# Kernel tuning notes

Hardware: AMD Instinct MI355X
Metric: run time of the kernel (lower is better)

Reference implementation:

```python
import jax, jax.numpy as jnp
import numpy as np

D = 1024
H = 16
HD = D // H
FF = 4096
B, S = 2, 2048


def _ln(x, g, b, eps):
    mu = jnp.mean(x, axis=-1, keepdims=True)
    var = jnp.mean(jnp.square(x - mu), axis=-1, keepdims=True)
    return (x - mu) * jax.lax.rsqrt(var + eps) * g + b


def setup_inputs() -> dict:
    key = jax.random.key(0)
    ks = jax.random.split(key, 12)
    s = 0.02
    return {
        "x": jax.random.normal(ks[0], (B, S, D), jnp.float32),
        "attention_mask": jnp.ones((B, 1, 1, S), jnp.int32),
        "wq": jax.random.normal(ks[1], (D, D), jnp.float32) * s,
        "bq": jnp.zeros((D,), jnp.float32),
        "wk": jax.random.normal(ks[2], (D, D), jnp.float32) * s,
        "bk": jnp.zeros((D,), jnp.float32),
        "wv": jax.random.normal(ks[3], (D, D), jnp.float32) * s,
        "bv": jnp.zeros((D,), jnp.float32),
        "wo": jax.random.normal(ks[4], (D, D), jnp.float32) * s,
        "bo": jnp.zeros((D,), jnp.float32),
        "ln1_g": jnp.ones((D,), jnp.float32),
        "ln1_b": jnp.zeros((D,), jnp.float32),
        "w1": jax.random.normal(ks[5], (D, FF), jnp.float32) * s,
        "b1": jnp.zeros((FF,), jnp.float32),
        "w2": jax.random.normal(ks[6], (FF, D), jnp.float32) * s,
        "b2": jnp.zeros((D,), jnp.float32),
        "lnf_g": jnp.ones((D,), jnp.float32),
        "lnf_b": jnp.zeros((D,), jnp.float32),
        "ln2_g": jnp.ones((D,), jnp.float32),
        "ln2_b": jnp.zeros((D,), jnp.float32),
    }


def reference(x, attention_mask, wq, bq, wk, bk, wv, bv, wo, bo,
              ln1_g, ln1_b, w1, b1, w2, b2, lnf_g, lnf_b, ln2_g, ln2_b):
    b, s, d = x.shape
    # --- naive multi-head self-attention ---
    q = (x @ wq + bq).reshape(b, s, H, HD).transpose(0, 2, 1, 3)  # [b,h,s,hd]
    k = (x @ wk + bk).reshape(b, s, H, HD).transpose(0, 2, 1, 3)
    v = (x @ wv + bv).reshape(b, s, H, HD).transpose(0, 2, 1, 3)
    scores = jnp.einsum('bhqd,bhkd->bhqk', q, k) / jnp.sqrt(jnp.float32(HD))
    scores = jnp.where(attention_mask == 0, jnp.float32(-1e9), scores)
    attn = jax.nn.softmax(scores, axis=-1)
    ctx = jnp.einsum('bhqk,bhkd->bhqd', attn, v)
    ctx = ctx.transpose(0, 2, 1, 3).reshape(b, s, d)
    attn_out = ctx @ wo + bo
    # residual + LayerNorm (eps=1e-5, torch default)
    x1 = _ln(x + attn_out, ln1_g, ln1_b, 1e-5)
    # --- BERT-style FFN with internal residual LN (eps=1e-12) ---
    h = jax.nn.gelu(x1 @ w1 + b1, approximate=False)
    ff = _ln(h @ w2 + b2 + x1, lnf_g, lnf_b, 1e-12)
    # --- outer residual + LayerNorm (eps=1e-5) ---
    return _ln(x1 + ff, ln2_g, ln2_b, 1e-5)
```

## Files before the change

kernel.cpp:

```cpp
#include <hip/hip_runtime.h>

#define DMODEL 1024
#define NHEAD  16
#define HDIM   64
#define FFDIM  4096
#define BATCH  2
#define SEQ    2048
#define MTOK   (BATCH*SEQ)

typedef __bf16 bf16;
typedef __bf16 bf16x8 __attribute__((ext_vector_type(8)));
typedef __bf16 bf16x4 __attribute__((ext_vector_type(4)));
typedef float  floatx4 __attribute__((ext_vector_type(4)));
typedef unsigned int u32;
typedef unsigned int u32x4 __attribute__((ext_vector_type(4)));

__device__ __forceinline__ int get_flag(const void* ln1g) {
  return (((const u32*)ln1g)[0] == 0x3F800000u) ? 0 : 1;
}
__device__ __forceinline__ float ld_ext(const void* p, size_t i, int flag) {
  return flag ? (float)((const bf16*)p)[i] : ((const float*)p)[i];
}

__device__ __forceinline__ void gload16(const bf16* g, bf16* lds_uniform) {
// ... 35 lines not shown
  }
  if (bid >= 12288) {
    size_t base = (size_t)(bid - 12288) * 1024;
    int i = threadIdx.x * 4;
    #pragma unroll
    for (int j = 0; j < 4; j++) xC[base + i + j] = (bf16)ld_ext(x, base + i + j, flag);
    return;
  }
  __shared__ bf16 tile[32][33];
  const void* in; bf16* out; int K, N, t;
  if      (bid < 1024)  { in = wq; out = WTqkv;                 K = 1024; N = 1024; t = bid; }
  else if (bid < 2048)  { in = wk; out = WTqkv + 1024 * 1024;   K = 1024; N = 1024; t = bid - 1024; }
  else if (bid < 3072)  { in = wv; out = WTqkv + 2 * 1024 * 1024; K = 1024; N = 1024; t = bid - 2048; }
  else if (bid < 4096)  { in = wo; out = WToT;                  K = 1024; N = 1024; t = bid - 3072; }
  else if (bid < 8192)  { in = w1; out = WT1;                   K = 1024; N = 4096; t = bid - 4096; }
  else                  { in = w2; out = WT2;                   K = 4096; N = 1024; t = bid - 8192; }
  int shift = (N == 4096) ? 7 : 5;
  int k0 = (t >> shift) * 32, n0 = (t & ((1 << shift) - 1)) * 32;
  int tx = threadIdx.x & 31, ty = threadIdx.x >> 5;
  #pragma unroll
  for (int i = ty; i < 32; i += 8)
    tile[i][tx] = (bf16)ld_ext(in, (size_t)(k0 + i) * N + n0 + tx, flag);
  __syncthreads();
  #pragma unroll
  for (int i = ty; i < 32; i += 8)
    out[(size_t)(n0 + i) * K + k0 + tx] = tile[tx][i];
}

__global__ __launch_bounds__(256) void gemm128(
    const bf16* __restrict__ A, const bf16* __restrict__ BT,
    const void* __restrict__ bias0, const void* __restrict__ bias1,
    const void* __restrict__ bias2,
    bf16* __restrict__ out0, bf16* __restrict__ out1, bf16* __restrict__ out2,
    int N, int K, int ksub, int mode, const void* __restrict__ ln1g)
{
  __shared__ __align__(16) char smem[32768];
  bf16* As = (bf16*)smem;
  bf16* Bs = (bf16*)(smem + 16384);
  int flag = get_flag(ln1g);

  int tid = threadIdx.x, lane = tid & 63, w = tid >> 6;
  int wm = w & 1, wn = w >> 1;
  int m0 = blockIdx.x * 128, n0 = blockIdx.y * 128;
  int kstart = blockIdx.z * ksub;
  int r15 = lane & 15, kg = lane >> 4;

  floatx4 acc[4][4];
  #pragma unroll
  for (int mt = 0; mt < 4; mt++)
    #pragma unroll
    for (int nt = 0; nt < 4; nt++) acc[mt][nt] = (floatx4){0.f, 0.f, 0.f, 0.f};

  int srow8 = lane >> 3;
  int skc = (lane & 7) ^ (srow8 & 7);
  const bf16* Ap = A  + (size_t)(m0 + w * 32 + srow8) * K + kstart + skc * 8;
  const bf16* Bp = BT + (size_t)(n0 + w * 32 + srow8) * K + kstart + skc * 8;
  const size_t jstr = (size_t)8 * K;

  for (int it = ksub >> 6; it > 0; it--) {
    #pragma unroll
    for (int j = 0; j < 4; j++) {
      gload16(Ap + j * jstr, As + (size_t)(w * 256 + j * 64) * 8);
      gload16(Bp + j * jstr, Bs + (size_t)(w * 256 + j * 64) * 8);
    }
    Ap += 64; Bp += 64;
    __syncthreads();

// ... 32 lines not shown
  for (int nt = 0; nt < 4; nt++) {
    int gcol = gcb + nt * 16 + r15;
    int bidx = (mode == 1) ? (gcol & 1023) : gcol;
    const void* bp = (mode == 1) ? ((which == 0) ? bias0 : (which == 1) ? bias1 : bias2) : bias0;
    bvs[nt] = (blockIdx.z == 0) ? ld_ext(bp, bidx, flag) : 0.f;
  }

  #pragma unroll
  for (int pass = 0; pass < 2; pass++) {
    #pragma unroll
    for (int mh = 0; mh < 2; mh++) {
      int mt = 2 * pass + mh;
      #pragma unroll
      for (int nt = 0; nt < 4; nt++) {
        int lcol = nt * 16 + r15;
        #pragma unroll
        for (int r = 0; r < 4; r++) {
          int lrow = mh * 16 + kg * 4 + r;
          float val = acc[mt][nt][r] + bvs[nt];
          if (mode == 2) val = gelu_f(val);
          if (mode == 1 && which == 0) val *= 0.125f;
          if (mode == 1 && which == 2) scr[lcol * 40 + lrow] = (bf16)val;
          else                         scr[lrow * 68 + lcol] = (bf16)val;
        }
      }
    }
    if (mode == 1 && which == 2) {
      int hh = (gcb - 2048) >> 6;
      int b = rowg0 >> 11, s0 = rowg0 & 2047;
      #pragma unroll
      for (int it = 0; it < 4; it++) {
        int c = it * 64 + lane;
        int cc = c >> 2, part = c & 3;
        bf16x8 vdat = *(const bf16x8*)&scr[cc * 40 + part * 8];
        *(bf16x8*)(out2 + ((size_t)(b * NHEAD + hh) * HDIM + cc) * SEQ + s0 + pass * 32 + part * 8) = vdat;
      }
    } else {
      #pragma unroll
      for (int it = 0; it < 4; it++) {
        int c = it * 64 + lane;
        int rr = c >> 3, part = c & 7;
        bf16x8 vdat = *(const bf16x8*)&scr[rr * 68 + part * 8];
        int rowg = rowg0 + pass * 32 + rr;
        bf16* dst;
        if (mode == 1) {
          int b = rowg >> 11, s = rowg & 2047;
          int hh = (gcb & 1023) >> 6;
          bf16* o = (which == 0) ? out0 : out1;
          dst = o + ((size_t)(b * NHEAD + hh) * SEQ + s) * HDIM + part * 8;
        } else {
          dst = outp + (size_t)rowg * N + gcb + part * 8;
        }
        *(bf16x8*)dst = vdat;
      }
    }
  }
}

#define STAGE_A(dstbuf, koff, qm)                                             \
  { int gch = (lane & 7) ^ (srow8 & 7);                                       \
    _Pragma("unroll") for (int j = 0; j < 2; j++) {                           \
      int rb = (qm) * 64 + j * 128 + w * 8;                                   \
      gload16(A + (size_t)(m0 + rb + srow8) * K + (koff) + gch * 8,           \
              (dstbuf) + (size_t)rb * 64);                                    \
    } }

#define STAGE_B(dstbuf, koff, qn)                                             \
  { int gch = (lane & 7) ^ (srow8 & 7);                                       \
    _Pragma("unroll") for (int j = 0; j < 2; j++) {                           \
      int rb = (2 * j + (w >> 2)) * 64 + (qn) * 32 + (w & 3) * 8;             \
      gload16(BT + (size_t)(n0 + rb + srow8) * K + (koff) + gch * 8,          \
              (dstbuf) + (size_t)rb * 64);                                    \
    } }

#define RD_A(QM)                                                              \
  _Pragma("unroll") for (int mt = 0; mt < 4; mt++) {                          \
    int row = wm * 128 + (QM) * 64 + mt * 16 + r15;                           \
    _Pragma("unroll") for (int kk = 0; kk < 2; kk++) {                        \
      int slot = (kk * 4 + kg) ^ (r15 & 7);                                   \
      af[mt][kk] = *(const bf16x8*)&Ac[(size_t)(row * 8 + slot) * 8];         \
    }                                                                         \
  }

#define RD_B(QN)                                                              \
  _Pragma("unroll") for (int nt = 0; nt < 2; nt++) {                          \
    int row = wn * 64 + (QN) * 32 + nt * 16 + r15;                            \
    _Pragma("unroll") for (int kk = 0; kk < 2; kk++) {                        \
      int slot = (kk * 4 + kg) ^ (r15 & 7);                                   \
      bfv[nt][kk] = *(const bf16x8*)&Bc[(size_t)(row * 8 + slot) * 8];        \
    }                                                                         \
  }

#define MF(QM, QN)                                                            \
  __builtin_amdgcn_s_setprio(1);                                              \
  _Pragma("unroll") for (int kk = 0; kk < 2; kk++)                            \
    _Pragma("unroll") for (int mt = 0; mt < 4; mt++)                          \
      _Pragma("unroll") for (int nt = 0; nt < 2; nt++)                        \
        acc[(QM) * 4 + mt][(QN) * 2 + nt] =                                   \
            __builtin_amdgcn_mfma_f32_16x16x32_bf16(                          \
                af[mt][kk], bfv[nt][kk],                                      \
                acc[(QM) * 4 + mt][(QN) * 2 + nt], 0, 0, 0);                  \
  __builtin_amdgcn_s_setprio(0);

__global__ __launch_bounds__(512, 2) void gemm256(
    const bf16* __restrict__ A, const bf16* __restrict__ BT,
    const void* __restrict__ bias0, bf16* __restrict__ out0,
    int N, int K, int ksub, int mode, const void* __restrict__ ln1g)
{
  __shared__ __align__(16) char smem[131072];
  int flag = get_flag(ln1g);

  int tid = threadIdx.x, lane = tid & 63, w = tid >> 6;
  int wm = w >> 2, wn = w & 3;
  int r15 = lane & 15, kg = lane >> 4;
  int srow8 = lane >> 3;

  int nx = gridDim.x, ny = gridDim.y;
  int nwg = nx * ny * gridDim.z;
  int wg = blockIdx.x + nx * (blockIdx.y + ny * blockIdx.z);
  if ((nwg & 7) == 0) wg = (wg & 7) * (nwg >> 3) + (wg >> 3);
  int bx = wg % nx, rem = wg / nx;
  int by = rem % ny, bz = rem / ny;

  int m0 = bx * 256, n0 = by * 256;
  int kstart = bz * ksub;
  int NT = ksub >> 6;

  floatx4 acc[8][4];
  #pragma unroll
  for (int mt = 0; mt < 8; mt++)
    #pragma unroll
    for (int nt = 0; nt < 4; nt++) acc[mt][nt] = (floatx4){0.f, 0.f, 0.f, 0.f};

  STAGE_A((bf16*)smem,             kstart, 0);
  STAGE_B((bf16*)(smem + 65536),   kstart, 0);
  STAGE_A((bf16*)smem,             kstart, 1);
  STAGE_B((bf16*)(smem + 65536),   kstart, 1);
  VMW(4);
  BAR();

  for (int t = 0; t < NT; t++) {
    int cur = (t & 1) * 32768, nxt = ((t + 1) & 1) * 32768;
    bf16* Ac = (bf16*)(smem + cur);
    bf16* Bc = (bf16*)(smem + 65536 + cur);
    bf16* An = (bf16*)(smem + nxt);
    bf16* Bn = (bf16*)(smem + 65536 + nxt);
    int t1 = (t + 1 < NT) ? t + 1 : NT - 1;
    int k1 = kstart + t1 * 64;

    bf16x8 af[4][2], bfv[2][2];
    RD_A(0); RD_B(0);
    STAGE_A(An, k1, 0);
    VMW(4);
    BAR(); MF(0, 0); BAR();
    RD_A(1);
    STAGE_B(Bn, k1, 0);
    VMW(4);
    BAR(); MF(1, 0); BAR();
    RD_B(1);
    STAGE_A(An, k1, 1);
    BAR(); MF(1, 1); BAR();
    RD_A(0);
    STAGE_B(Bn, k1, 1);
    VMW(4);
    BAR(); MF(0, 1); BAR();
  }

  VMW(0);
  BAR();

  bf16* scr = (bf16*)(smem + 5120 * w);
  int gcb = n0 + wn * 64;
  int rowg0 = m0 + wm * 128;
  bf16* outp = out0 + (size_t)bz * MTOK * (size_t)N;

  float bvs[4];
  #pragma unroll
  for (int nt = 0; nt < 4; nt++) {
    int gcol = gcb + nt * 16 + r15;
    bvs[nt] = (bz == 0) ? ld_ext(bias0, gcol, flag) : 0.f;
  }

  #pragma unroll
  for (int pass = 0; pass < 4; pass++) {
    #pragma unroll
    for (int mh = 0; mh < 2; mh++) {
      int mt = 2 * pass + mh;
      #pragma unroll
      for (int nt = 0; nt < 4; nt++) {
        #pragma unroll
        for (int r = 0; r < 4; r++) {
          int lrow = mh * 16 + kg * 4 + r;
          float val = acc[mt][nt][r] + bvs[nt];
          if (mode == 2) val = gelu_f(val);
          scr[lrow * 68 + nt * 16 + r15] = (bf16)val;
        }
      }
    }
    #pragma unroll
    for (int it = 0; it < 4; it++) {
      int c = it * 64 + lane;
      int rr = c >> 3, part = c & 7;
      bf16x8 vdat = *(const bf16x8*)&scr[rr * 68 + part * 8];
      int rowg = rowg0 + pass * 32 + rr;
      *(bf16x8*)(outp + (size_t)rowg * N + gcb + part * 8) = vdat;
    }
  }
}

__global__ __launch_bounds__(256) void attn_mfma(
    const bf16* __restrict__ q, const bf16* __restrict__ k,
    const bf16* __restrict__ vt, const u32* __restrict__ mwAll,
    const bf16* __restrict__ m01All, bf16* __restrict__ ctx)
{
  __shared__ __align__(16) bf16 Ks[2][4096];
  __shared__ __align__(16) bf16 Vts[2][4096];
  __shared__ __align__(16) bf16 Ps[4][2048];

  int tid = threadIdx.x, lane = tid & 63, w = tid >> 6;
  int r15 = lane & 15, kg = lane >> 4;
  int x7 = r15 & 7;
  int bh = (blockIdx.x & 7) * 4 + ((blockIdx.x >> 3) >> 4);
  int qt = (blockIdx.x >> 3) & 15;
  int b = bh >> 4, h = bh & 15;
  int q0 = qt * 128 + w * 32;

  bf16x8 qf[2][2];
  #pragma unroll
  for (int mt = 0; mt < 2; mt++)
    #pragma unroll
    for (int kt2 = 0; kt2 < 2; kt2++)
      qf[mt][kt2] = *(const bf16x8*)(q + ((size_t)bh * SEQ + q0 + mt * 16 + r15) * HDIM + kt2 * 32 + kg * 8);

  floatx4 O[2][4];
  floatx4 lacc[2];
  #pragma unroll
  for (int mt = 0; mt < 2; mt++) {
    lacc[mt] = (floatx4){0.f, 0.f, 0.f, 0.f};
    #pragma unroll
    for (int dt = 0; dt < 4; dt++) O[mt][dt] = (floatx4){0.f, 0.f, 0.f, 0.f};
  }

  int slo = kg ^ x7, shi = (kg + 4) ^ x7;
  const bf16* pap[2][2];
  #pragma unroll
  for (int mt = 0; mt < 2; mt++) {
    pap[mt][0] = &Ps[w][((mt * 16 + r15) * 8 + slo) * 8];
    pap[mt][1] = &Ps[w][((mt * 16 + r15) * 8 + shi) * 8];
  }

  int kr = lane >> 3, kc = lane & 7;
  int vrow = tid >> 3, vcc = tid & 7;
  int vsw = vcc ^ (vrow & 7);
  const bf16* kb_ = k + (size_t)bh * SEQ * HDIM;
  const bf16* vb_ = vt + (size_t)bh * HDIM * SEQ;
  const u32*  mwb = mwAll + (size_t)b * (SEQ / 2);
  const bf16* m1b = m01All + (size_t)b * SEQ;

  u32x4 pv0 = *(const u32x4*)(vb_ + (size_t)vrow * SEQ + vcc * 8);
  u32x4 pv1 = *(const u32x4*)(vb_ + (size_t)(vrow + 32) * SEQ + vcc * 8);
  u32x4 pmw = *(const u32x4*)&mwb[vcc * 4];
  bf16x8 m0c = *(const bf16x8*)&m1b[kg * 8];
  bf16x8 m1c = *(const bf16x8*)&m1b[32 + kg * 8];
  asm volatile("" ::: "memory");
  #pragma unroll
  for (int j = 0; j < 2; j++)
    gload16(kb_ + (size_t)(16 * w + 8 * j + kr) * HDIM + (kc ^ kr) * 8,
            &Ks[0][0] + (size_t)(w * 128 + j * 64) * 8);
  VMW(4);
  pv0 &= pmw; pv1 &= pmw;
  *(u32x4*)&Vts[0][(vrow * 8 + vsw) * 8] = pv0;
  *(u32x4*)&Vts[0][((vrow + 32) * 8 + vsw) * 8] = pv1;
  asm volatile("s_waitcnt lgkmcnt(0)" ::: "memory");
  __builtin_amdgcn_s_barrier();
  asm volatile("" ::: "memory");

  for (int t = 0; t < SEQ / 64; t++) {
    int cur = t & 1, nxt = cur ^ 1;
    int ktn = (t + 1 < SEQ / 64) ? (t + 1) * 64 : t * 64;
    u32x4 nv0 = *(const u32x4*)(vb_ + (size_t)vrow * SEQ + ktn + vcc * 8);
    u32x4 nv1 = *(const u32x4*)(vb_ + (size_t)(vrow + 32) * SEQ + ktn + vcc * 8);
    u32x4 nmw = *(const u32x4*)&mwb[(ktn + vcc * 8) >> 1];
    bf16x8 nm0 = *(const bf16x8*)&m1b[ktn + kg * 8];
    bf16x8 nm1 = *(const bf16x8*)&m1b[ktn + 32 + kg * 8];
    asm volatile("" ::: "memory");
    #pragma unroll
    for (int j = 0; j < 2; j++)
      gload16(kb_ + (size_t)(ktn + 16 * w + 8 * j + kr) * HDIM + (kc ^ kr) * 8,
              &Ks[nxt][0] + (size_t)(w * 128 + j * 64) * 8);
    VMW(7);
    __builtin_amdgcn_s_barrier();
    asm volatile("" ::: "memory");

    const bf16* Kc = &Ks[cur][0];
    const bf16* Vc = &Vts[cur][0];

    floatx4 S[2][4];
    #pragma unroll
    for (int mt = 0; mt < 2; mt++)
      #pragma unroll
      for (int nt = 0; nt < 4; nt++) S[mt][nt] = (floatx4){0.f, 0.f, 0.f, 0.f};
    __builtin_amdgcn_s_setprio(1);
    #pragma unroll
    for (int nt = 0; nt < 4; nt++) {
      int rb = (nt * 16 + r15) * 8;
      bf16x8 kf0 = *(const bf16x8*)&Kc[(rb + slo) * 8];
      bf16x8 kf1 = *(const bf16x8*)&Kc[(rb + shi) * 8];
      #pragma unroll
      for (int mt = 0; mt < 2; mt++) {
        S[mt][nt] = __builtin_amdgcn_mfma_f32_16x16x32_bf16(kf0, qf[mt][0], S[mt][nt], 0, 0, 0);
        S[mt][nt] = __builtin_amdgcn_mfma_f32_16x16x32_bf16(kf1, qf[mt][1], S[mt][nt], 0, 0, 0);
      }
    }
    __builtin_amdgcn_s_setprio(0);

    #pragma unroll
    for (int mt = 0; mt < 2; mt++)
      #pragma unroll
      for (int nt = 0; nt < 4; nt++) {
        bf16x4 pk;
        #pragma unroll
        for (int r = 0; r < 4; r++) pk[r] = (bf16)__expf(S[mt][nt][r]);
        int c2 = 2 * nt + (kg >> 1);
        *(bf16x4*)&Ps[w][((mt * 16 + r15) * 8 + (c2 ^ x7)) * 8 + (kg & 1) * 4] = pk;
      }

    bf16x8 pa[2][2];
    #pragma unroll
    for (int mt = 0; mt < 2; mt++) {
      pa[mt][0] = *(const bf16x8*)pap[mt][0];
      pa[mt][1] = *(const bf16x8*)pap[mt][1];
    }
    __builtin_amdgcn_s_setprio(1);
    #pragma unroll
    for (int dt = 0; dt < 4; dt++) {
      int rb = (dt * 16 + r15) * 8;
      bf16x8 vf0 = *(const bf16x8*)&Vc[(rb + slo) * 8];
      bf16x8 vf1 = *(const bf16x8*)&Vc[(rb + shi) * 8];
      #pragma unroll
      for (int mt = 0; mt < 2; mt++) {
        O[mt][dt] = __builtin_amdgcn_mfma_f32_16x16x32_bf16(pa[mt][0], vf0, O[mt][dt], 0, 0, 0);
        O[mt][dt] = __builtin_amdgcn_mfma_f32_16x16x32_bf16(pa[mt][1], vf1, O[mt][dt], 0, 0, 0);
      }
    }
    #pragma unroll
    for (int mt = 0; mt < 2; mt++) {
      lacc[mt] = __builtin_amdgcn_mfma_f32_16x16x32_bf16(pa[mt][0], m0c, lacc[mt], 0, 0, 0);
      lacc[mt] = __builtin_amdgcn_mfma_f32_16x16x32_bf16(pa[mt][1], m1c, lacc[mt], 0, 0, 0);
    }
    __builtin_amdgcn_s_setprio(0);

    VMW(2);
    nv0 &= nmw; nv1 &= nmw;
    *(u32x4*)&Vts[nxt][(vrow * 8 + vsw) * 8] = nv0;
    *(u32x4*)&Vts[nxt][((vrow + 32) * 8 + vsw) * 8] = nv1;
    m0c = nm0; m1c = nm1;
    asm volatile("s_waitcnt lgkmcnt(0)" ::: "memory");
    __builtin_amdgcn_s_barrier();
    asm volatile("" ::: "memory");
  }
  VMW(0);

  #pragma unroll
  for (int mt = 0; mt < 2; mt++) {
    float inv[4];
    #pragma unroll
    for (int r = 0; r < 4; r++) inv[r] = 1.f / lacc[mt][r];
    #pragma unroll
    for (int dt = 0; dt < 4; dt++)
      #pragma unroll
      for (int r = 0; r < 4; r++) {
        int srow = q0 + mt * 16 + kg * 4 + r;
        int col = h * 64 + dt * 16 + r15;
        ctx[((size_t)b * SEQ + srow) * DMODEL + col] = (bf16)(O[mt][dt][r] * inv[r]);
      }
  }
}

__global__ __launch_bounds__(256) void ln_kernel(
    const bf16* ba, const bf16* bb, const bf16* bc,
    const void* g, const void* be, float eps, bf16* outb, const void* ln1g)
{
  __shared__ float red1[4], red2[4];
  int flag = get_flag(ln1g);
  size_t base = (size_t)blockIdx.x * DMODEL;
  float v[4];
  #pragma unroll
  for (int i = 0; i < 4; i++) {
    int idx = threadIdx.x + i * 256;
    v[i] = (float)ba[base + idx] + (float)bb[base + idx] + (float)bc[base + idx];
  }
  float sum = v[0] + v[1] + v[2] + v[3];
  #pragma unroll
  for (int o = 32; o > 0; o >>= 1) sum += __shfl_xor(sum, o);
  if ((threadIdx.x & 63) == 0) red1[threadIdx.x >> 6] = sum;
  __syncthreads();
  float mean = (red1[0] + red1[1] + red1[2] + red1[3]) * (1.f / DMODEL);
  float sq = 0.f;
  #pragma unroll
  for (int i = 0; i < 4; i++) { v[i] -= mean; sq += v[i] * v[i]; }
  #pragma unroll
  for (int o = 32; o > 0; o >>= 1) sq += __shfl_xor(sq, o);
  if ((threadIdx.x & 63) == 0) red2[threadIdx.x >> 6] = sq;
  __syncthreads();
  float rstd = rsqrtf((red2[0] + red2[1] + red2[2] + red2[3]) * (1.f / DMODEL) + eps);
  #pragma unroll
  for (int i = 0; i < 4; i++) {
    int idx = threadIdx.x + i * 256;
    outb[base + idx] = (bf16)(v[i] * rstd * ld_ext(g, idx, flag) + ld_ext(be, idx, flag));
// ... 57 lines not shown
    int idx = threadIdx.x + i * 256;
    float y = v[i] * rstd * ld_ext(g2, idx, flag) + ld_ext(b2, idx, flag);
    if (flag) ((bf16*)out_ext)[base + idx] = (bf16)y;
    else      ((float*)out_ext)[base + idx] = y;
  }
}

extern "C" void kernel_launch(void* const* d_in, const int* in_sizes, int n_in,
                              void* d_out, int out_size, void* d_ws, size_t ws_size,
                              hipStream_t stream) {
  const void* x    = d_in[0];
  const int*  msk  = (const int*)d_in[1];
  const void* wq   = d_in[2];
  const void* bq   = d_in[3];
  const void* wk   = d_in[4];
  const void* bk   = d_in[5];
  const void* wv   = d_in[6];
  const void* bv   = d_in[7];
  const void* wo   = d_in[8];
  const void* bo   = d_in[9];
  const void* ln1g = d_in[10];
  const void* ln1b = d_in[11];
  const void* w1   = d_in[12];
  const void* b1   = d_in[13];
  const void* w2   = d_in[14];
  const void* b2   = d_in[15];
  const void* lnfg = d_in[16];
  const void* lnfb = d_in[17];
  const void* ln2g = d_in[18];
  const void* ln2b = d_in[19];

  const size_t MB = 1024 * 1024;
  char* p = (char*)d_ws;
  int big = ws_size >= (size_t)80 * MB;
  bf16* xC     = (bf16*)(p + 0 * MB);
  bf16* qb     = (bf16*)(p + 8 * MB);
  bf16* kb     = (bf16*)(p + 16 * MB);
  bf16* vtb    = (bf16*)(p + 24 * MB);
  bf16* ctxb   = (bf16*)(p + 32 * MB);
  bf16* WTqkv  = (bf16*)(p + 40 * MB);
  bf16* WToT   = (bf16*)(p + 46 * MB);
  bf16* WT1    = (bf16*)(p + 48 * MB);
  bf16* WT2    = (bf16*)(p + (big ? 72 : 56) * MB);
  bf16* ao     = (bf16*)(p + 8 * MB);
  bf16* x1b    = xC;
  bf16* hb     = (bf16*)(p + 8 * MB);
  bf16* ffp    = (bf16*)(p + 40 * MB);
  u32*  mwAll  = (u32*)d_out;
  bf16* m01All = (bf16*)((char*)d_out + 8192);
  const size_t PS = (size_t)MTOK * DMODEL;

  prep<<<16386, 256, 0, stream>>>(wq, wk, wv, wo, w1, w2, x, msk,
                                  WTqkv, WToT, WT1, WT2, xC, mwAll, m01All, ln1g);

  gemm128<<<dim3(MTOK / 128, 3072 / 128, 1), 256, 0, stream>>>(
      xC, WTqkv, bq, bk, bv, qb, kb, vtb, 3072, DMODEL, DMODEL, 1, ln1g);

  attn_mfma<<<BATCH * NHEAD * (SEQ / 128), 256, 0, stream>>>(qb, kb, vtb, mwAll, m01All, ctxb);

  gemm128<<<dim3(MTOK / 128, DMODEL / 128, 2), 256, 0, stream>>>(
      ctxb, WToT, bo, nullptr, nullptr, ao, nullptr, nullptr, DMODEL, DMODEL, 512, 3, ln1g);

  ln_kernel<<<MTOK, 256, 0, stream>>>(ao, ao + PS, xC, ln1g, ln1b,
                                      1e-5f, x1b, ln1g);

  gemm256<<<dim3(MTOK / 256, FFDIM / 256, 1), 512, 0, stream>>>(
      x1b, WT1, b1, hb, FFDIM, DMODEL, DMODEL, 2, ln1g);

  if (big) {
    gemm256<<<dim3(MTOK / 256, DMODEL / 256, 4), 512, 0, stream>>>(
        hb, WT2, b2, ffp, DMODEL, FFDIM, FFDIM / 4, 3, ln1g);
    ln_double<<<MTOK, 256, 0, stream>>>(ffp, ffp + PS, ffp + 2 * PS, ffp + 3 * PS,
                                        x1b, lnfg, lnfb, ln2g, ln2b, d_out, ln1g, 4);
  } else {
    gemm128<<<dim3(MTOK / 128, DMODEL / 128, 2), 256, 0, stream>>>(
        hb, WT2, b2, nullptr, nullptr, ffp, nullptr, nullptr, DMODEL, FFDIM, 2048, 3, ln1g);
    ln_double<<<MTOK, 256, 0, stream>>>(ffp, ffp + PS, ffp, ffp,
                                        x1b, lnfg, lnfb, ln2g, ln2b, d_out, ln1g, 2);
  }
}
```

Before: 358.9 us.

## Load K/V fragments directly from global in attention, move V masking into QKV GEMM

The attention kernel no longer stages K and V tiles through double-buffered LDS with barriers. Each wave now loads its K and V MFMA fragments directly from global memory, which removes the LDS traffic and the per-iteration block barriers. The mask multiply on V moves into the QKV GEMM epilogue, which writes V already masked. The cost is redundant global/L2 reads, since all four waves now load the same K/V tiles, and there is no explicit prefetch of the next tile.

```diff
diff --git a/kernel.cpp b/kernel.cpp
--- a/kernel.cpp
+++ b/kernel.cpp
@@ -91,7 +91,8 @@
     const void* __restrict__ bias0, const void* __restrict__ bias1,
     const void* __restrict__ bias2,
     bf16* __restrict__ out0, bf16* __restrict__ out1, bf16* __restrict__ out2,
-    int N, int K, int ksub, int mode, const void* __restrict__ ln1g)
+    int N, int K, int ksub, int mode, const void* __restrict__ ln1g,
+    const u32* __restrict__ mwAll)
 {
   __shared__ __align__(16) char smem[32768];
   bf16* As = (bf16*)smem;
@@ -190,8 +191,10 @@
       for (int it = 0; it < 4; it++) {
         int c = it * 64 + lane;
         int cc = c >> 2, part = c & 3;
-        bf16x8 vdat = *(const bf16x8*)&scr[cc * 40 + part * 8];
-        *(bf16x8*)(out2 + ((size_t)(b * NHEAD + hh) * HDIM + cc) * SEQ + s0 + pass * 32 + part * 8) = vdat;
+        u32x4 vv = *(const u32x4*)&scr[cc * 40 + part * 8];
+        int scol = s0 + pass * 32 + part * 8;
+        vv &= *(const u32x4*)&mwAll[(size_t)b * (SEQ / 2) + (scol >> 1)];
+        *(u32x4*)(out2 + ((size_t)(b * NHEAD + hh) * HDIM + cc) * SEQ + scol) = vv;
       }
     } else {
       #pragma unroll
@@ -368,11 +371,9 @@
 
 __global__ __launch_bounds__(256) void attn_mfma(
     const bf16* __restrict__ q, const bf16* __restrict__ k,
-    const bf16* __restrict__ vt, const u32* __restrict__ mwAll,
-    const bf16* __restrict__ m01All, bf16* __restrict__ ctx)
+    const bf16* __restrict__ vt, const bf16* __restrict__ m01All,
+    bf16* __restrict__ ctx)
 {
-  __shared__ __align__(16) bf16 Ks[2][4096];
-  __shared__ __align__(16) bf16 Vts[2][4096];
   __shared__ __align__(16) bf16 Ps[4][2048];
 
   int tid = threadIdx.x, lane = tid & 63, w = tid >> 6;
@@ -387,8 +388,8 @@
   #pragma unroll
   for (int mt = 0; mt < 2; mt++)
     #pragma unroll
-    for (int kt2 = 0; kt2 < 2; kt2++)
-      qf[mt][kt2] = *(const bf16x8*)(q + ((size_t)bh * SEQ + q0 + mt * 16 + r15) * HDIM + kt2 * 32 + kg * 8);
+    for (int k2 = 0; k2 < 2; k2++)
+      qf[mt][k2] = *(const bf16x8*)(q + ((size_t)bh * SEQ + q0 + mt * 16 + r15) * HDIM + k2 * 32 + kg * 8);
 
   floatx4 O[2][4];
   floatx4 lacc[2];
@@ -407,51 +408,25 @@
     pap[mt][1] = &Ps[w][((mt * 16 + r15) * 8 + shi) * 8];
   }
 
-  int kr = lane >> 3, kc = lane & 7;
-  int vrow = tid >> 3, vcc = tid & 7;
-  int vsw = vcc ^ (vrow & 7);
   const bf16* kb_ = k + (size_t)bh * SEQ * HDIM;
   const bf16* vb_ = vt + (size_t)bh * HDIM * SEQ;
-  const u32*  mwb = mwAll + (size_t)b * (SEQ / 2);
   const bf16* m1b = m01All + (size_t)b * SEQ;
 
-  u32x4 pv0 = *(const u32x4*)(vb_ + (size_t)vrow * SEQ + vcc * 8);
-  u32x4 pv1 = *(const u32x4*)(vb_ + (size_t)(vrow + 32) * SEQ + vcc * 8);
-  u32x4 pmw = *(const u32x4*)&mwb[vcc * 4];
-  bf16x8 m0c = *(const bf16x8*)&m1b[kg * 8];
-  bf16x8 m1c = *(const bf16x8*)&m1b[32 + kg * 8];
-  asm volatile("" ::: "memory");
-  #pragma unroll
-  for (int j = 0; j < 2; j++)
-    gload16(kb_ + (size_t)(16 * w + 8 * j + kr) * HDIM + (kc ^ kr) * 8,
-            &Ks[0][0] + (size_t)(w * 128 + j * 64) * 8);
-  VMW(4);
-  pv0 &= pmw; pv1 &= pmw;
-  *(u32x4*)&Vts[0][(vrow * 8 + vsw) * 8] = pv0;
-  *(u32x4*)&Vts[0][((vrow + 32) * 8 + vsw) * 8] = pv1;
-  asm volatile("s_waitcnt lgkmcnt(0)" ::: "memory");
-  __builtin_amdgcn_s_barrier();
-  asm volatile("" ::: "memory");
-
   for (int t = 0; t < SEQ / 64; t++) {
-    int cur = t & 1, nxt = cur ^ 1;
-    int ktn = (t + 1 < SEQ / 64) ? (t + 1) * 64 : t * 64;
-    u32x4 nv0 = *(const u32x4*)(vb_ + (size_t)vrow * SEQ + ktn + vcc * 8);
-    u32x4 nv1 = *(const u32x4*)(vb_ + (size_t)(vrow + 32) * SEQ + ktn + vcc * 8);
-    u32x4 nmw = *(const u32x4*)&mwb[(ktn + vcc * 8) >> 1];
-    bf16x8 nm0 = *(const bf16x8*)&m1b[ktn + kg * 8];
-    bf16x8 nm1 = *(const bf16x8*)&m1b[ktn + 32 + kg * 8];
-    asm volatile("" ::: "memory");
-    #pragma unroll
-    for (int j = 0; j < 2; j++)
-      gload16(kb_ + (size_t)(ktn + 16 * w + 8 * j + kr) * HDIM + (kc ^ kr) * 8,
-              &Ks[nxt][0] + (size_t)(w * 128 + j * 64) * 8);
-    VMW(7);
-    __builtin_amdgcn_s_barrier();
-    asm volatile("" ::: "memory");
-
-    const bf16* Kc = &Ks[cur][0];
-    const bf16* Vc = &Vts[cur][0];
+    int kt = t * 64;
+    bf16x8 kf[4][2], vf[4][2];
+    #pragma unroll
+    for (int nt = 0; nt < 4; nt++)
+      #pragma unroll
+      for (int k2 = 0; k2 < 2; k2++)
+        kf[nt][k2] = *(const bf16x8*)(kb_ + (size_t)(kt + nt * 16 + r15) * HDIM + k2 * 32 + kg * 8);
+    #pragma unroll
+    for (int dt = 0; dt < 4; dt++)
+      #pragma unroll
+      for (int hf = 0; hf < 2; hf++)
+        vf[dt][hf] = *(const bf16x8*)(vb_ + (size_t)(dt * 16 + r15) * SEQ + kt + hf * 32 + kg * 8);
+    bf16x8 m0c = *(const bf16x8*)&m1b[kt + kg * 8];
+    bf16x8 m1c = *(const bf16x8*)&m1b[kt + 32 + kg * 8];
 
     floatx4 S[2][4];
     #pragma unroll
@@ -460,16 +435,12 @@
       for (int nt = 0; nt < 4; nt++) S[mt][nt] = (floatx4){0.f, 0.f, 0.f, 0.f};
     __builtin_amdgcn_s_setprio(1);
     #pragma unroll
-    for (int nt = 0; nt < 4; nt++) {
-      int rb = (nt * 16 + r15) * 8;
-      bf16x8 kf0 = *(const bf16x8*)&Kc[(rb + slo) * 8];
-      bf16x8 kf1 = *(const bf16x8*)&Kc[(rb + shi) * 8];
+    for (int nt = 0; nt < 4; nt++)
       #pragma unroll
       for (int mt = 0; mt < 2; mt++) {
-        S[mt][nt] = __builtin_amdgcn_mfma_f32_16x16x32_bf16(kf0, qf[mt][0], S[mt][nt], 0, 0, 0);
-        S[mt][nt] = __builtin_amdgcn_mfma_f32_16x16x32_bf16(kf1, qf[mt][1], S[mt][nt], 0, 0, 0);
-      }
-    }
+        S[mt][nt] = __builtin_amdgcn_mfma_f32_16x16x32_bf16(kf[nt][0], qf[mt][0], S[mt][nt], 0, 0, 0);
+        S[mt][nt] = __builtin_amdgcn_mfma_f32_16x16x32_bf16(kf[nt][1], qf[mt][1], S[mt][nt], 0, 0, 0);
+      }
     __builtin_amdgcn_s_setprio(0);
 
     #pragma unroll
@@ -491,33 +462,19 @@
     }
     __builtin_amdgcn_s_setprio(1);
     #pragma unroll
-    for (int dt = 0; dt < 4; dt++) {
-      int rb = (dt * 16 + r15) * 8;
-      bf16x8 vf0 = *(const bf16x8*)&Vc[(rb + slo) * 8];
-      bf16x8 vf1 = *(const bf16x8*)&Vc[(rb + shi) * 8];
+    for (int dt = 0; dt < 4; dt++)
       #pragma unroll
       for (int mt = 0; mt < 2; mt++) {
-        O[mt][dt] = __builtin_amdgcn_mfma_f32_16x16x32_bf16(pa[mt][0], vf0, O[mt][dt], 0, 0, 0);
-        O[mt][dt] = __builtin_amdgcn_mfma_f32_16x16x32_bf16(pa[mt][1], vf1, O[mt][dt], 0, 0, 0);
-      }
-    }
+        O[mt][dt] = __builtin_amdgcn_mfma_f32_16x16x32_bf16(pa[mt][0], vf[dt][0], O[mt][dt], 0, 0, 0);
+        O[mt][dt] = __builtin_amdgcn_mfma_f32_16x16x32_bf16(pa[mt][1], vf[dt][1], O[mt][dt], 0, 0, 0);
+      }
     #pragma unroll
     for (int mt = 0; mt < 2; mt++) {
       lacc[mt] = __builtin_amdgcn_mfma_f32_16x16x32_bf16(pa[mt][0], m0c, lacc[mt], 0, 0, 0);
       lacc[mt] = __builtin_amdgcn_mfma_f32_16x16x32_bf16(pa[mt][1], m1c, lacc[mt], 0, 0, 0);
     }
     __builtin_amdgcn_s_setprio(0);
-
-    VMW(2);
-    nv0 &= nmw; nv1 &= nmw;
-    *(u32x4*)&Vts[nxt][(vrow * 8 + vsw) * 8] = nv0;
-    *(u32x4*)&Vts[nxt][((vrow + 32) * 8 + vsw) * 8] = nv1;
-    m0c = nm0; m1c = nm1;
-    asm volatile("s_waitcnt lgkmcnt(0)" ::: "memory");
-    __builtin_amdgcn_s_barrier();
-    asm volatile("" ::: "memory");
-  }
-  VMW(0);
+  }
 
   #pragma unroll
   for (int mt = 0; mt < 2; mt++) {
@@ -678,12 +635,12 @@
                                   WTqkv, WToT, WT1, WT2, xC, mwAll, m01All, ln1g);
 
   gemm128<<<dim3(MTOK / 128, 3072 / 128, 1), 256, 0, stream>>>(
-      xC, WTqkv, bq, bk, bv, qb, kb, vtb, 3072, DMODEL, DMODEL, 1, ln1g);
-
-  attn_mfma<<<BATCH * NHEAD * (SEQ / 128), 256, 0, stream>>>(qb, kb, vtb, mwAll, m01All, ctxb);
+      xC, WTqkv, bq, bk, bv, qb, kb, vtb, 3072, DMODEL, DMODEL, 1, ln1g, mwAll);
+
+  attn_mfma<<<BATCH * NHEAD * (SEQ / 128), 256, 0, stream>>>(qb, kb, vtb, m01All, ctxb);
 
   gemm128<<<dim3(MTOK / 128, DMODEL / 128, 2), 256, 0, stream>>>(
-      ctxb, WToT, bo, nullptr, nullptr, ao, nullptr, nullptr, DMODEL, DMODEL, 512, 3, ln1g);
+      ctxb, WToT, bo, nullptr, nullptr, ao, nullptr, nullptr, DMODEL, DMODEL, 512, 3, ln1g, nullptr);
 
   ln_kernel<<<MTOK, 256, 0, stream>>>(ao, ao + PS, xC, ln1g, ln1b,
                                       1e-5f, x1b, ln1g);
@@ -698,7 +655,7 @@
                                         x1b, lnfg, lnfb, ln2g, ln2b, d_out, ln1g, 4);
   } else {
     gemm128<<<dim3(MTOK / 128, DMODEL / 128, 2), 256, 0, stream>>>(
-        hb, WT2, b2, nullptr, nullptr, ffp, nullptr, nullptr, DMODEL, FFDIM, 2048, 3, ln1g);
+        hb, WT2, b2, nullptr, nullptr, ffp, nullptr, nullptr, DMODEL, FFDIM, 2048, 3, ln1g, nullptr);
     ln_double<<<MTOK, 256, 0, stream>>>(ffp, ffp + PS, ffp, ffp,
                                         x1b, lnfg, lnfb, ln2g, ln2b, d_out, ln1g, 2);
   }
```

Measured after the change: 444.3 us. +23.8%, slower.

## Split attention over the key dimension and move V masking into the QKV epilogue

Applied to the files above, without the earlier changes.

The attention kernel gains a second grid dimension that splits the key/value sequence into halves. Each half writes its unnormalized partial context and row sums, and a new combine kernel adds the halves and normalizes. This doubles the block count to improve CU occupancy and load balance, at the cost of an extra pass over ctx-sized buffers and bf16 rounding of the partial outputs. The attention-mask multiply on V is also moved into the QKV GEMM epilogue, which removes per-tile mask-word loads from the attention inner loop. The split path runs only when the workspace is at least 90 MB.

```diff
diff --git a/kernel.cpp b/kernel.cpp
--- a/kernel.cpp
+++ b/kernel.cpp
@@ -91,7 +91,8 @@
     const void* __restrict__ bias0, const void* __restrict__ bias1,
     const void* __restrict__ bias2,
     bf16* __restrict__ out0, bf16* __restrict__ out1, bf16* __restrict__ out2,
-    int N, int K, int ksub, int mode, const void* __restrict__ ln1g)
+    int N, int K, int ksub, int mode, const void* __restrict__ ln1g,
+    const u32* __restrict__ mwAll)
 {
   __shared__ __align__(16) char smem[32768];
   bf16* As = (bf16*)smem;
@@ -190,8 +191,10 @@
       for (int it = 0; it < 4; it++) {
         int c = it * 64 + lane;
         int cc = c >> 2, part = c & 3;
-        bf16x8 vdat = *(const bf16x8*)&scr[cc * 40 + part * 8];
-        *(bf16x8*)(out2 + ((size_t)(b * NHEAD + hh) * HDIM + cc) * SEQ + s0 + pass * 32 + part * 8) = vdat;
+        u32x4 vv = *(const u32x4*)&scr[cc * 40 + part * 8];
+        int scol = s0 + pass * 32 + part * 8;
+        vv &= *(const u32x4*)&mwAll[(size_t)b * (SEQ / 2) + (scol >> 1)];
+        *(u32x4*)(out2 + ((size_t)(b * NHEAD + hh) * HDIM + cc) * SEQ + scol) = vv;
       }
     } else {
       #pragma unroll
@@ -368,8 +371,8 @@
 
 __global__ __launch_bounds__(256) void attn_mfma(
     const bf16* __restrict__ q, const bf16* __restrict__ k,
-    const bf16* __restrict__ vt, const u32* __restrict__ mwAll,
-    const bf16* __restrict__ m01All, bf16* __restrict__ ctx)
+    const bf16* __restrict__ vt, const bf16* __restrict__ m01All,
+    bf16* __restrict__ ctx, bf16* __restrict__ p1, float* __restrict__ laccO)
 {
   __shared__ __align__(16) bf16 Ks[2][4096];
   __shared__ __align__(16) bf16 Vts[2][4096];
@@ -382,6 +385,8 @@
   int qt = (blockIdx.x >> 3) & 15;
   int b = bh >> 4, h = bh & 15;
   int q0 = qt * 128 + w * 32;
+  int nz = gridDim.y, z = blockIdx.y;
+  int tA = (SEQ / 64 / nz) * z, tB = tA + SEQ / 64 / nz;
 
   bf16x8 qf[2][2];
   #pragma unroll
@@ -412,33 +417,30 @@
   int vsw = vcc ^ (vrow & 7);
   const bf16* kb_ = k + (size_t)bh * SEQ * HDIM;
   const bf16* vb_ = vt + (size_t)bh * HDIM * SEQ;
-  const u32*  mwb = mwAll + (size_t)b * (SEQ / 2);
   const bf16* m1b = m01All + (size_t)b * SEQ;
 
-  u32x4 pv0 = *(const u32x4*)(vb_ + (size_t)vrow * SEQ + vcc * 8);
-  u32x4 pv1 = *(const u32x4*)(vb_ + (size_t)(vrow + 32) * SEQ + vcc * 8);
-  u32x4 pmw = *(const u32x4*)&mwb[vcc * 4];
-  bf16x8 m0c = *(const bf16x8*)&m1b[kg * 8];
-  bf16x8 m1c = *(const bf16x8*)&m1b[32 + kg * 8];
+  int kt0 = tA * 64;
+  u32x4 pv0 = *(const u32x4*)(vb_ + (size_t)vrow * SEQ + kt0 + vcc * 8);
+  u32x4 pv1 = *(const u32x4*)(vb_ + (size_t)(vrow + 32) * SEQ + kt0 + vcc * 8);
+  bf16x8 m0c = *(const bf16x8*)&m1b[kt0 + kg * 8];
+  bf16x8 m1c = *(const bf16x8*)&m1b[kt0 + 32 + kg * 8];
   asm volatile("" ::: "memory");
   #pragma unroll
   for (int j = 0; j < 2; j++)
-    gload16(kb_ + (size_t)(16 * w + 8 * j + kr) * HDIM + (kc ^ kr) * 8,
+    gload16(kb_ + (size_t)(kt0 + 16 * w + 8 * j + kr) * HDIM + (kc ^ kr) * 8,
             &Ks[0][0] + (size_t)(w * 128 + j * 64) * 8);
   VMW(4);
-  pv0 &= pmw; pv1 &= pmw;
   *(u32x4*)&Vts[0][(vrow * 8 + vsw) * 8] = pv0;
   *(u32x4*)&Vts[0][((vrow + 32) * 8 + vsw) * 8] = pv1;
   asm volatile("s_waitcnt lgkmcnt(0)" ::: "memory");
   __builtin_amdgcn_s_barrier();
   asm volatile("" ::: "memory");
 
-  for (int t = 0; t < SEQ / 64; t++) {
-    int cur = t & 1, nxt = cur ^ 1;
-    int ktn = (t + 1 < SEQ / 64) ? (t + 1) * 64 : t * 64;
+  for (int t = tA; t < tB; t++) {
+    int cur = (t - tA) & 1, nxt = cur ^ 1;
+    int ktn = (t + 1 < tB) ? (t + 1) * 64 : t * 64;
     u32x4 nv0 = *(const u32x4*)(vb_ + (size_t)vrow * SEQ + ktn + vcc * 8);
     u32x4 nv1 = *(const u32x4*)(vb_ + (size_t)(vrow + 32) * SEQ + ktn + vcc * 8);
-    u32x4 nmw = *(const u32x4*)&mwb[(ktn + vcc * 8) >> 1];
     bf16x8 nm0 = *(const bf16x8*)&m1b[ktn + kg * 8];
     bf16x8 nm1 = *(const bf16x8*)&m1b[ktn + 32 + kg * 8];
     asm volatile("" ::: "memory");
@@ -446,7 +448,7 @@
     for (int j = 0; j < 2; j++)
       gload16(kb_ + (size_t)(ktn + 16 * w + 8 * j + kr) * HDIM + (kc ^ kr) * 8,
               &Ks[nxt][0] + (size_t)(w * 128 + j * 64) * 8);
-    VMW(7);
+    VMW(6);
     __builtin_amdgcn_s_barrier();
     asm volatile("" ::: "memory");
 
@@ -509,7 +511,6 @@
     __builtin_amdgcn_s_setprio(0);
 
     VMW(2);
-    nv0 &= nmw; nv1 &= nmw;
     *(u32x4*)&Vts[nxt][(vrow * 8 + vsw) * 8] = nv0;
     *(u32x4*)&Vts[nxt][((vrow + 32) * 8 + vsw) * 8] = nv1;
     m0c = nm0; m1c = nm1;
@@ -519,20 +520,58 @@
   }
   VMW(0);
 
-  #pragma unroll
-  for (int mt = 0; mt < 2; mt++) {
-    float inv[4];
-    #pragma unroll
-    for (int r = 0; r < 4; r++) inv[r] = 1.f / lacc[mt][r];
-    #pragma unroll
-    for (int dt = 0; dt < 4; dt++)
-      #pragma unroll
-      for (int r = 0; r < 4; r++) {
-        int srow = q0 + mt * 16 + kg * 4 + r;
-        int col = h * 64 + dt * 16 + r15;
-        ctx[((size_t)b * SEQ + srow) * DMODEL + col] = (bf16)(O[mt][dt][r] * inv[r]);
-      }
-  }
+  if (nz == 1) {
+    #pragma unroll
+    for (int mt = 0; mt < 2; mt++) {
+      float inv[4];
+      #pragma unroll
+      for (int r = 0; r < 4; r++) inv[r] = 1.f / lacc[mt][r];
+      #pragma unroll
+      for (int dt = 0; dt < 4; dt++)
+        #pragma unroll
+        for (int r = 0; r < 4; r++) {
+          int srow = q0 + mt * 16 + kg * 4 + r;
+          int col = h * 64 + dt * 16 + r15;
+          ctx[((size_t)b * SEQ + srow) * DMODEL + col] = (bf16)(O[mt][dt][r] * inv[r]);
+        }
+    }
+  } else {
+    bf16* po = (z == 0) ? ctx : p1;
+    #pragma unroll
+    for (int mt = 0; mt < 2; mt++) {
+      #pragma unroll
+      for (int dt = 0; dt < 4; dt++)
+        #pragma unroll
+        for (int r = 0; r < 4; r++) {
+          int srow = q0 + mt * 16 + kg * 4 + r;
+          int col = h * 64 + dt * 16 + r15;
+          po[((size_t)b * SEQ + srow) * DMODEL + col] = (bf16)O[mt][dt][r];
+        }
+      if (r15 == 0) {
+        #pragma unroll
+        for (int r = 0; r < 4; r++)
+          laccO[((size_t)z * NHEAD * BATCH + bh) * SEQ + q0 + mt * 16 + kg * 4 + r] = lacc[mt][r];
+      }
+    }
+  }
+}
+
+__global__ __launch_bounds__(256) void attn_combine(
+    bf16* ctx, const bf16* p1, const float* laccO)
+{
+  int row = blockIdx.x;
+  int b = row >> 11, s = row & 2047;
+  int c0 = threadIdx.x * 4;
+  int h = c0 >> 6;
+  size_t li = (size_t)(b * NHEAD + h) * SEQ + s;
+  float inv = 1.f / (laccO[li] + laccO[(size_t)NHEAD * BATCH * SEQ + li]);
+  size_t base = (size_t)row * DMODEL + c0;
+  bf16x4 a = *(const bf16x4*)&ctx[base];
+  bf16x4 bb = *(const bf16x4*)&p1[base];
+  bf16x4 o;
+  #pragma unroll
+  for (int j = 0; j < 4; j++) o[j] = (bf16)(((float)a[j] + (float)bb[j]) * inv);
+  *(bf16x4*)&ctx[base] = o;
 }
 
 __global__ __launch_bounds__(256) void ln_kernel(
@@ -656,7 +695,8 @@
 
   const size_t MB = 1024 * 1024;
   char* p = (char*)d_ws;
-  int big = ws_size >= (size_t)80 * MB;
+  int big  = ws_size >= (size_t)80 * MB;
+  int big2 = ws_size >= (size_t)90 * MB;
   bf16* xC     = (bf16*)(p + 0 * MB);
   bf16* qb     = (bf16*)(p + 8 * MB);
   bf16* kb     = (bf16*)(p + 16 * MB);
@@ -666,6 +706,8 @@
   bf16* WToT   = (bf16*)(p + 46 * MB);
   bf16* WT1    = (bf16*)(p + 48 * MB);
   bf16* WT2    = (bf16*)(p + (big ? 72 : 56) * MB);
+  bf16* aP1    = (bf16*)(p + 80 * MB);
+  float* aL    = (float*)(p + 88 * MB);
   bf16* ao     = (bf16*)(p + 8 * MB);
   bf16* x1b    = xC;
   bf16* hb     = (bf16*)(p + 8 * MB);
@@ -678,12 +720,19 @@
                                   WTqkv, WToT, WT1, WT2, xC, mwAll, m01All, ln1g);
 
   gemm128<<<dim3(MTOK / 128, 3072 / 128, 1), 256, 0, stream>>>(
-      xC, WTqkv, bq, bk, bv, qb, kb, vtb, 3072, DMODEL, DMODEL, 1, ln1g);
-
-  attn_mfma<<<BATCH * NHEAD * (SEQ / 128), 256, 0, stream>>>(qb, kb, vtb, mwAll, m01All, ctxb);
+      xC, WTqkv, bq, bk, bv, qb, kb, vtb, 3072, DMODEL, DMODEL, 1, ln1g, mwAll);
+
+  if (big2) {
+    attn_mfma<<<dim3(BATCH * NHEAD * (SEQ / 128), 2), 256, 0, stream>>>(
+        qb, kb, vtb, m01All, ctxb, aP1, aL);
+    attn_combine<<<MTOK, 256, 0, stream>>>(ctxb, aP1, aL);
+  } else {
+    attn_mfma<<<dim3(BATCH * NHEAD * (SEQ / 128), 1), 256, 0, stream>>>(
+        qb, kb, vtb, m01All, ctxb, ctxb, aL);
+  }
 
   gemm128<<<dim3(MTOK / 128, DMODEL / 128, 2), 256, 0, stream>>>(
-      ctxb, WToT, bo, nullptr, nullptr, ao, nullptr, nullptr, DMODEL, DMODEL, 512, 3, ln1g);
+      ctxb, WToT, bo, nullptr, nullptr, ao, nullptr, nullptr, DMODEL, DMODEL, 512, 3, ln1g, nullptr);
 
   ln_kernel<<<MTOK, 256, 0, stream>>>(ao, ao + PS, xC, ln1g, ln1b,
                                       1e-5f, x1b, ln1g);
@@ -698,7 +747,7 @@
                                         x1b, lnfg, lnfb, ln2g, ln2b, d_out, ln1g, 4);
   } else {
     gemm128<<<dim3(MTOK / 128, DMODEL / 128, 2), 256, 0, stream>>>(
-        hb, WT2, b2, nullptr, nullptr, ffp, nullptr, nullptr, DMODEL, FFDIM, 2048, 3, ln1g);
+        hb, WT2, b2, nullptr, nullptr, ffp, nullptr, nullptr, DMODEL, FFDIM, 2048, 3, ln1g, nullptr);
     ln_double<<<MTOK, 256, 0, stream>>>(ffp, ffp + PS, ffp, ffp,
                                         x1b, lnfg, lnfb, ln2g, ln2b, d_out, ln1g, 2);
   }
```

Result: slower. 386.5 us (+7.7%).

## Restructure gemm256 main loop to two barriers-free halves; move V mask into QKV epilogue

Applied to the files above, without the earlier changes.

The gemm256 K-loop is restructured. B fragments are read once per step, A is read in two halves, and both A stages are issued before the first MFMA block. The four barrier-separated MFMA quarters become two setprio blocks with a single wait and barrier per iteration. Separately, the attention-mask AND on V moves from the attention kernel's inner loop into the QKV GEMM epilogue, which removes one global load and two ANDs per attention tile. The risk is less overlap of global loads with compute, since the loop now waits for all loads (VMW(0)) every iteration, and more fragment registers are live at once.

```diff
diff --git a/kernel.cpp b/kernel.cpp
--- a/kernel.cpp
+++ b/kernel.cpp
@@ -91,7 +91,8 @@
     const void* __restrict__ bias0, const void* __restrict__ bias1,
     const void* __restrict__ bias2,
     bf16* __restrict__ out0, bf16* __restrict__ out1, bf16* __restrict__ out2,
-    int N, int K, int ksub, int mode, const void* __restrict__ ln1g)
+    int N, int K, int ksub, int mode, const void* __restrict__ ln1g,
+    const u32* __restrict__ mwAll)
 {
   __shared__ __align__(16) char smem[32768];
   bf16* As = (bf16*)smem;
@@ -190,8 +191,10 @@
       for (int it = 0; it < 4; it++) {
         int c = it * 64 + lane;
         int cc = c >> 2, part = c & 3;
-        bf16x8 vdat = *(const bf16x8*)&scr[cc * 40 + part * 8];
-        *(bf16x8*)(out2 + ((size_t)(b * NHEAD + hh) * HDIM + cc) * SEQ + s0 + pass * 32 + part * 8) = vdat;
+        u32x4 vv = *(const u32x4*)&scr[cc * 40 + part * 8];
+        int scol = s0 + pass * 32 + part * 8;
+        vv &= *(const u32x4*)&mwAll[(size_t)b * (SEQ / 2) + (scol >> 1)];
+        *(u32x4*)(out2 + ((size_t)(b * NHEAD + hh) * HDIM + cc) * SEQ + scol) = vv;
       }
     } else {
       #pragma unroll
@@ -231,34 +234,32 @@
               (dstbuf) + (size_t)rb * 64);                                    \
     } }
 
-#define RD_A(QM)                                                              \
+#define RD_AQ(QM)                                                             \
   _Pragma("unroll") for (int mt = 0; mt < 4; mt++) {                          \
     int row = wm * 128 + (QM) * 64 + mt * 16 + r15;                           \
     _Pragma("unroll") for (int kk = 0; kk < 2; kk++) {                        \
       int slot = (kk * 4 + kg) ^ (r15 & 7);                                   \
-      af[mt][kk] = *(const bf16x8*)&Ac[(size_t)(row * 8 + slot) * 8];         \
+      av[mt][kk] = *(const bf16x8*)&Ac[(size_t)(row * 8 + slot) * 8];         \
     }                                                                         \
   }
 
-#define RD_B(QN)                                                              \
-  _Pragma("unroll") for (int nt = 0; nt < 2; nt++) {                          \
-    int row = wn * 64 + (QN) * 32 + nt * 16 + r15;                            \
+#define RD_BF()                                                               \
+  _Pragma("unroll") for (int j = 0; j < 4; j++) {                             \
+    int row = wn * 64 + j * 16 + r15;                                         \
     _Pragma("unroll") for (int kk = 0; kk < 2; kk++) {                        \
       int slot = (kk * 4 + kg) ^ (r15 & 7);                                   \
-      bfv[nt][kk] = *(const bf16x8*)&Bc[(size_t)(row * 8 + slot) * 8];        \
+      bv4[j][kk] = *(const bf16x8*)&Bc[(size_t)(row * 8 + slot) * 8];         \
     }                                                                         \
   }
 
-#define MF(QM, QN)                                                            \
-  __builtin_amdgcn_s_setprio(1);                                              \
+#define MF2(QM, QN)                                                           \
   _Pragma("unroll") for (int kk = 0; kk < 2; kk++)                            \
     _Pragma("unroll") for (int mt = 0; mt < 4; mt++)                          \
       _Pragma("unroll") for (int nt = 0; nt < 2; nt++)                        \
         acc[(QM) * 4 + mt][(QN) * 2 + nt] =                                   \
             __builtin_amdgcn_mfma_f32_16x16x32_bf16(                          \
-                af[mt][kk], bfv[nt][kk],                                      \
-                acc[(QM) * 4 + mt][(QN) * 2 + nt], 0, 0, 0);                  \
-  __builtin_amdgcn_s_setprio(0);
+                av[mt][kk], bv4[(QN) * 2 + nt][kk],                           \
+                acc[(QM) * 4 + mt][(QN) * 2 + nt], 0, 0, 0);
 
 __global__ __launch_bounds__(512, 2) void gemm256(
     const bf16* __restrict__ A, const bf16* __restrict__ BT,
@@ -291,10 +292,10 @@
     for (int nt = 0; nt < 4; nt++) acc[mt][nt] = (floatx4){0.f, 0.f, 0.f, 0.f};
 
   STAGE_A((bf16*)smem,             kstart, 0);
+  STAGE_A((bf16*)smem,             kstart, 1);
   STAGE_B((bf16*)(smem + 65536),   kstart, 0);
-  STAGE_A((bf16*)smem,             kstart, 1);
   STAGE_B((bf16*)(smem + 65536),   kstart, 1);
-  VMW(4);
+  VMW(0);
   BAR();
 
   for (int t = 0; t < NT; t++) {
@@ -306,26 +307,24 @@
     int t1 = (t + 1 < NT) ? t + 1 : NT - 1;
     int k1 = kstart + t1 * 64;
 
-    bf16x8 af[4][2], bfv[2][2];
-    RD_A(0); RD_B(0);
+    bf16x8 av[4][2], bv4[4][2];
+    RD_BF();
+    RD_AQ(0);
     STAGE_A(An, k1, 0);
-    VMW(4);
-    BAR(); MF(0, 0); BAR();
-    RD_A(1);
+    STAGE_A(An, k1, 1);
+    __builtin_amdgcn_s_setprio(1);
+    MF2(0, 0); MF2(0, 1);
+    __builtin_amdgcn_s_setprio(0);
+    RD_AQ(1);
     STAGE_B(Bn, k1, 0);
-    VMW(4);
-    BAR(); MF(1, 0); BAR();
-    RD_B(1);
-    STAGE_A(An, k1, 1);
-    BAR(); MF(1, 1); BAR();
-    RD_A(0);
     STAGE_B(Bn, k1, 1);
-    VMW(4);
-    BAR(); MF(0, 1); BAR();
-  }
-
-  VMW(0);
-  BAR();
+    __builtin_amdgcn_s_setprio(1);
+    MF2(1, 0); MF2(1, 1);
+    __builtin_amdgcn_s_setprio(0);
+    VMW(0);
+    BAR();
+  }
+
 
   bf16* scr = (bf16*)(smem + 5120 * w);
   int gcb = n0 + wn * 64;
@@ -368,8 +367,8 @@
 
 __global__ __launch_bounds__(256) void attn_mfma(
     const bf16* __restrict__ q, const bf16* __restrict__ k,
-    const bf16* __restrict__ vt, const u32* __restrict__ mwAll,
-    const bf16* __restrict__ m01All, bf16* __restrict__ ctx)
+    const bf16* __restrict__ vt, const bf16* __restrict__ m01All,
+    bf16* __restrict__ ctx)
 {
   __shared__ __align__(16) bf16 Ks[2][4096];
   __shared__ __align__(16) bf16 Vts[2][4096];
@@ -412,12 +411,10 @@
   int vsw = vcc ^ (vrow & 7);
   const bf16* kb_ = k + (size_t)bh * SEQ * HDIM;
   const bf16* vb_ = vt + (size_t)bh * HDIM * SEQ;
-  const u32*  mwb = mwAll + (size_t)b * (SEQ / 2);
   const bf16* m1b = m01All + (size_t)b * SEQ;
 
   u32x4 pv0 = *(const u32x4*)(vb_ + (size_t)vrow * SEQ + vcc * 8);
   u32x4 pv1 = *(const u32x4*)(vb_ + (size_t)(vrow + 32) * SEQ + vcc * 8);
-  u32x4 pmw = *(const u32x4*)&mwb[vcc * 4];
   bf16x8 m0c = *(const bf16x8*)&m1b[kg * 8];
   bf16x8 m1c = *(const bf16x8*)&m1b[32 + kg * 8];
   asm volatile("" ::: "memory");
@@ -426,7 +423,6 @@
     gload16(kb_ + (size_t)(16 * w + 8 * j + kr) * HDIM + (kc ^ kr) * 8,
             &Ks[0][0] + (size_t)(w * 128 + j * 64) * 8);
   VMW(4);
-  pv0 &= pmw; pv1 &= pmw;
   *(u32x4*)&Vts[0][(vrow * 8 + vsw) * 8] = pv0;
   *(u32x4*)&Vts[0][((vrow + 32) * 8 + vsw) * 8] = pv1;
   asm volatile("s_waitcnt lgkmcnt(0)" ::: "memory");
@@ -438,7 +434,6 @@
     int ktn = (t + 1 < SEQ / 64) ? (t + 1) * 64 : t * 64;
     u32x4 nv0 = *(const u32x4*)(vb_ + (size_t)vrow * SEQ + ktn + vcc * 8);
     u32x4 nv1 = *(const u32x4*)(vb_ + (size_t)(vrow + 32) * SEQ + ktn + vcc * 8);
-    u32x4 nmw = *(const u32x4*)&mwb[(ktn + vcc * 8) >> 1];
     bf16x8 nm0 = *(const bf16x8*)&m1b[ktn + kg * 8];
     bf16x8 nm1 = *(const bf16x8*)&m1b[ktn + 32 + kg * 8];
     asm volatile("" ::: "memory");
@@ -446,7 +441,7 @@
     for (int j = 0; j < 2; j++)
       gload16(kb_ + (size_t)(ktn + 16 * w + 8 * j + kr) * HDIM + (kc ^ kr) * 8,
               &Ks[nxt][0] + (size_t)(w * 128 + j * 64) * 8);
-    VMW(7);
+    VMW(6);
     __builtin_amdgcn_s_barrier();
     asm volatile("" ::: "memory");
 
@@ -509,7 +504,6 @@
     __builtin_amdgcn_s_setprio(0);
 
     VMW(2);
-    nv0 &= nmw; nv1 &= nmw;
     *(u32x4*)&Vts[nxt][(vrow * 8 + vsw) * 8] = nv0;
     *(u32x4*)&Vts[nxt][((vrow + 32) * 8 + vsw) * 8] = nv1;
     m0c = nm0; m1c = nm1;
@@ -678,12 +672,13 @@
                                   WTqkv, WToT, WT1, WT2, xC, mwAll, m01All, ln1g);
 
   gemm128<<<dim3(MTOK / 128, 3072 / 128, 1), 256, 0, stream>>>(
-      xC, WTqkv, bq, bk, bv, qb, kb, vtb, 3072, DMODEL, DMODEL, 1, ln1g);
-
-  attn_mfma<<<BATCH * NHEAD * (SEQ / 128), 256, 0, stream>>>(qb, kb, vtb, mwAll, m01All, ctxb);
+      xC, WTqkv, bq, bk, bv, qb, kb, vtb, 3072, DMODEL, DMODEL, 1, ln1g, mwAll);
+
+  attn_mfma<<<BATCH * NHEAD * (SEQ / 128), 256, 0, stream>>>(
+      qb, kb, vtb, m01All, ctxb);
 
   gemm128<<<dim3(MTOK / 128, DMODEL / 128, 2), 256, 0, stream>>>(
-      ctxb, WToT, bo, nullptr, nullptr, ao, nullptr, nullptr, DMODEL, DMODEL, 512, 3, ln1g);
+      ctxb, WToT, bo, nullptr, nullptr, ao, nullptr, nullptr, DMODEL, DMODEL, 512, 3, ln1g, nullptr);
 
   ln_kernel<<<MTOK, 256, 0, stream>>>(ao, ao + PS, xC, ln1g, ln1b,
                                       1e-5f, x1b, ln1g);
@@ -698,7 +693,7 @@
                                         x1b, lnfg, lnfb, ln2g, ln2b, d_out, ln1g, 4);
   } else {
     gemm128<<<dim3(MTOK / 128, DMODEL / 128, 2), 256, 0, stream>>>(
-        hb, WT2, b2, nullptr, nullptr, ffp, nullptr, nullptr, DMODEL, FFDIM, 2048, 3, ln1g);
+        hb, WT2, b2, nullptr, nullptr, ffp, nullptr, nullptr, DMODEL, FFDIM, 2048, 3, ln1g, nullptr);
     ln_double<<<MTOK, 256, 0, stream>>>(ffp, ffp + PS, ffp, ffp,
                                         x1b, lnfg, lnfb, ln2g, ln2b, d_out, ln1g, 2);
   }
```

Measured after the change: 368.1 us. 1.03x slower.
